# Performance work log

Hardware: AMD Instinct MI355X
Metric: run time of the kernel (lower is better)

The kernel has to match this reference:

```python
import jax, jax.numpy as jnp
import numpy as np

N_NODES = 50000
N_EDGES = 800000
F_IN = 512
HID = 256
N_CLS = 40
W_DIM = 50  # dimension*dimension*2 with dimension=5


def _prelu(x, a):
    return jnp.where(x >= 0, x, a * x)


def _segment_softmax(w, idx, n):
    # per-segment (grouped by idx), per-channel numerically stable softmax
    m = jax.ops.segment_max(w, idx, num_segments=n)
    e = jnp.exp(w - m[idx])
    s = jax.ops.segment_sum(e, idx, num_segments=n)
    return e / s[idx]


def _curvgn(x, edge_index, w_mul, W, b, w0, a, w1, b1):
    n = x.shape[0]
    h = x @ W + b                                   # [N, C]
    ow = _prelu(w_mul @ w0, a) @ w1 + b1            # [E, C] edge-weight MLP
    ow = _segment_softmax(ow, edge_index[0], n)     # softmax grouped by source (as in source)
    msg = ow * h[edge_index[0]]                     # gather x_j, weight
    return jax.ops.segment_sum(msg, edge_index[1], num_segments=n)  # scatter-add at target


def setup_inputs() -> dict:
    key = jax.random.key(0)
    ks = jax.random.split(key, 12)
    s = 0.05
    return {
        "x": jax.random.normal(ks[0], (N_NODES, F_IN), jnp.float32),
        "edge_index": jax.random.randint(ks[1], (2, N_EDGES), 0, N_NODES, jnp.int64 if jax.config.jax_enable_x64 else jnp.int32).astype(jnp.int32),
        "w_mul": jax.random.normal(ks[2], (N_EDGES, W_DIM), jnp.float32),
        "W1": jax.random.normal(ks[3], (F_IN, HID), jnp.float32) * s,
        "b1": jnp.zeros((HID,), jnp.float32),
        "m1_w0": jax.random.normal(ks[4], (W_DIM, HID), jnp.float32) * s,
        "m1_a": jnp.full((HID,), 0.2, jnp.float32),
        "m1_w1": jax.random.normal(ks[5], (HID, HID), jnp.float32) * s,
        "m1_b1": jnp.zeros((HID,), jnp.float32),
        "W2": jax.random.normal(ks[6], (HID, N_CLS), jnp.float32) * s,
        "b2": jnp.zeros((N_CLS,), jnp.float32),
        "m2_w0": jax.random.normal(ks[7], (W_DIM, N_CLS), jnp.float32) * s,
        "m2_a": jnp.full((N_CLS,), 0.2, jnp.float32),
        "m2_w1": jax.random.normal(ks[8], (N_CLS, N_CLS), jnp.float32) * s,
        "m2_b1": jnp.zeros((N_CLS,), jnp.float32),
    }


def reference(x, edge_index, w_mul, W1, b1, m1_w0, m1_a, m1_w1, m1_b1,
              W2, b2, m2_w0, m2_a, m2_w1, m2_b1):
    # eval mode: dropout is identity
    h = _curvgn(x, edge_index, w_mul, W1, b1, m1_w0, m1_a, m1_w1, m1_b1)
    h = jax.nn.elu(h)
    out = _curvgn(h, edge_index, w_mul, W2, b2, m2_w0, m2_a, m2_w1, m2_b1)
    return jax.nn.log_softmax(out, axis=1)
```

## Files before the change

kernel.cpp:

```cpp
#include <hip/hip_runtime.h>
#include <hip/hip_bf16.h>
#include <math.h>

#define N_NODESC 50000
#define N_EDGESC 800000
#define F_INC 512
#define HIDC 256
#define N_CLSC 40
#define W_DIMC 50
#define HN (2*N_NODESC)
#define NB_SCAN 196

typedef __bf16 bf16;
typedef __bf16 bf16x8 __attribute__((ext_vector_type(8)));
typedef __bf16 bf16x4 __attribute__((ext_vector_type(4)));
typedef __bf16 bf16x2 __attribute__((ext_vector_type(2)));
typedef float  f32x4  __attribute__((ext_vector_type(4)));
typedef float  f32x2  __attribute__((ext_vector_type(2)));

__global__ void k_hist(const int* __restrict__ ei, int* __restrict__ hist) {
    int e = blockIdx.x*256 + threadIdx.x;
    if (e < N_EDGESC) {
        atomicAdd(&hist[ei[e]], 1);
        atomicAdd(&hist[N_NODESC + ei[N_EDGESC + e]], 1);
    }
}
__global__ void k_copy(int* d, const int* s, int n) {
    int i = blockIdx.x*256 + threadIdx.x;
    if (i < n) d[i] = s[i];
}
__global__ void k_scan_part(const int* __restrict__ hist, int* __restrict__ part) {
    __shared__ int lds[512];
    int t = threadIdx.x;
    int i = blockIdx.x*512 + t;
    lds[t] = (i < HN) ? hist[i] : 0;
    __syncthreads();
    for (int off = 256; off > 0; off >>= 1) {
        if (t < off) lds[t] += lds[t+off];
        __syncthreads();
    }
    if (t == 0) part[blockIdx.x] = lds[0];
}
__global__ void k_scan_mid(const int* __restrict__ part, int* __restrict__ partx) {
    __shared__ int lds[256];
    int t = threadIdx.x;
    int v = (t < NB_SCAN) ? part[t] : 0;
    lds[t] = v;
    __syncthreads();
    for (int off = 1; off < 256; off <<= 1) {
        int add = (t >= off) ? lds[t-off] : 0;
        __syncthreads();
        lds[t] += add;
        __syncthreads();
    }
    partx[t] = lds[t] - v;
}
__global__ void k_scan_apply(const int* __restrict__ hist, const int* __restrict__ partx,
                             int* __restrict__ basev) {
    __shared__ int lds[512];
    int t = threadIdx.x;
    int i = blockIdx.x*512 + t;
    int v = (i < HN) ? hist[i] : 0;
    lds[t] = v;
    __syncthreads();
    for (int off = 1; off < 512; off <<= 1) {
        int add = (t >= off) ? lds[t-off] : 0;
        __syncthreads();
        lds[t] += add;
        __syncthreads();
    }
    if (i < HN) basev[i] = lds[t] - v + partx[blockIdx.x];
}
__global__ void k_scatter(const int* __restrict__ ei, int* __restrict__ cursor,
                          int* __restrict__ perm_src,
                          int* __restrict__ spd, int* __restrict__ svd) {
    int e = blockIdx.x*256 + threadIdx.x;
    if (e >= N_EDGESC) return;
    int s = ei[e];
    int d = ei[N_EDGESC + e];
    int p = atomicAdd(&cursor[s], 1);
    perm_src[p] = e;
    int q = atomicAdd(&cursor[N_NODESC + d], 1) - N_EDGESC;
    spd[q] = p;
    svd[q] = s;
}

__global__ void k_tconv(const float* __restrict__ src, bf16* __restrict__ dst,
                        int Ks, int Ns, int Kp, int Np) {
    int idx = blockIdx.x*256 + threadIdx.x;
    if (idx >= Kp*Np) return;
    int n = idx / Kp, k = idx - n*Kp;
    float v = (k < Ks && n < Ns) ? src[k*Ns + n] : 0.f;
    dst[idx] = (bf16)v;
}

__global__ __launch_bounds__(256) void k_h1(const float* __restrict__ x,
                                            const bf16* __restrict__ W1t,
                                            const float* __restrict__ b1,
                                            bf16* __restrict__ h1) {
    __shared__ __align__(16) bf16 a_lds[64*40];
    int tid = threadIdx.x;
    int lane = tid & 63, wv = tid >> 6;
    int l15 = lane & 15, quad = lane >> 4;
    int r0 = blockIdx.x * 64;
    f32x4 acc[4][4] = {};
    for (int ks = 0; ks < 16; ++ks) {
        #pragma unroll
        for (int i = 0; i < 2; ++i) {
            int idx = tid + i*256;
            int rl = idx >> 3, c4 = idx & 7;
            int rg = r0 + rl;
            f32x4 v = {};
            if (rg < N_NODESC) v = *(const f32x4*)&x[(size_t)rg*F_INC + ks*32 + c4*4];
            bf16x4 b; b[0]=(bf16)v[0]; b[1]=(bf16)v[1]; b[2]=(bf16)v[2]; b[3]=(bf16)v[3];
            *(bf16x4*)&a_lds[rl*40 + c4*4] = b;
        }
        __syncthreads();
        bf16x8 af[4], bfr[4];
        #pragma unroll
        for (int mt = 0; mt < 4; ++mt)
            af[mt] = *(const bf16x8*)&a_lds[(mt*16 + l15)*40 + quad*8];
        #pragma unroll
        for (int nt = 0; nt < 4; ++nt) {
            int n = wv*64 + nt*16 + l15;
            bfr[nt] = *(const bf16x8*)&W1t[n*F_INC + ks*32 + quad*8];
        }
        #pragma unroll
        for (int mt = 0; mt < 4; ++mt)
            #pragma unroll
            for (int nt = 0; nt < 4; ++nt)
                acc[mt][nt] = __builtin_amdgcn_mfma_f32_16x16x32_bf16(af[mt], bfr[nt], acc[mt][nt], 0, 0, 0);
        __syncthreads();
    }
    #pragma unroll
    for (int nt = 0; nt < 4; ++nt) {
        int col = wv*64 + nt*16 + l15;
        float bias = b1[col];
        #pragma unroll
        for (int mt = 0; mt < 4; ++mt)
            #pragma unroll
            for (int r = 0; r < 4; ++r) {
                int row = r0 + mt*16 + quad*4 + r;
                if (row < N_NODESC) h1[(size_t)row*HIDC + col] = (bf16)(acc[mt][nt][r] + bias);
            }
    }
}

__global__ __launch_bounds__(256) void k_mlp1(
    const float* __restrict__ w_mul, const int* __restrict__ perm_src,
    const int* __restrict__ ei,
    const bf16* __restrict__ w0t, const float* __restrict__ a1,
    const bf16* __restrict__ w1t, const float* __restrict__ bb1,
    bf16* __restrict__ eow1, float* __restrict__ s1) {
    __shared__ __align__(16) bf16 wm[64*72];
    __shared__ __align__(16) bf16 t1[64*264];
    __shared__ int e_lds[64], sv[64];
    int tid = threadIdx.x;
    int lane = tid & 63, wv = tid >> 6;
    int l15 = lane & 15, quad = lane >> 4;
    int p0 = blockIdx.x * 64;

    if (tid < 64) {
        int e = perm_src[p0 + tid];
        e_lds[tid] = e;
        sv[tid] = ei[e];
    }
    __syncthreads();
    #pragma unroll
    for (int i = 0; i < 7; ++i) {
        int idx = i*256 + tid;
        if (idx < 1600) {
            int row = idx / 25;
            int k = 2*(idx - row*25);
            f32x2 v = *(const f32x2*)&w_mul[(size_t)e_lds[row]*W_DIMC + k];
            bf16x2 b; b[0] = (bf16)v[0]; b[1] = (bf16)v[1];
            *(bf16x2*)&wm[row*72 + k] = b;
        }
    }
    #pragma unroll
    for (int i = 0; i < 2; ++i) {
        int idx = i*256 + tid;
        if (idx < 448) {
            int row = idx / 7, c = 50 + 2*(idx - row*7);
            bf16x2 z; z[0] = (bf16)0.f; z[1] = (bf16)0.f;
            *(bf16x2*)&wm[row*72 + c] = z;
        }
    }
    __syncthreads();

    {
        f32x4 acc[4][4] = {};
        bf16x8 af[2][4], bfr[2][4];
        #pragma unroll
        for (int ks = 0; ks < 2; ++ks) {
            #pragma unroll
            for (int mt = 0; mt < 4; ++mt)
                af[ks][mt] = *(const bf16x8*)&wm[(mt*16 + l15)*72 + ks*32 + quad*8];
            #pragma unroll
            for (int i = 0; i < 4; ++i)
                bfr[ks][i] = *(const bf16x8*)&w0t[(wv*64 + i*16 + l15)*64 + ks*32 + quad*8];
        }
        #pragma unroll
        for (int ks = 0; ks < 2; ++ks)
            #pragma unroll
            for (int mt = 0; mt < 4; ++mt)
                #pragma unroll
                for (int i = 0; i < 4; ++i)
                    acc[mt][i] = __builtin_amdgcn_mfma_f32_16x16x32_bf16(af[ks][mt], bfr[ks][i], acc[mt][i], 0, 0, 0);
        #pragma unroll
        for (int i = 0; i < 4; ++i) {
            int col = wv*64 + i*16 + l15;
            float al = a1[col];
            #pragma unroll
            for (int mt = 0; mt < 4; ++mt)
                #pragma unroll
                for (int r = 0; r < 4; ++r) {
                    float v = acc[mt][i][r];
                    v = (v >= 0.f) ? v : al*v;
                    t1[(mt*16 + quad*4 + r)*264 + col] = (bf16)v;
                }
        }
    }
    __syncthreads();

    {
        f32x4 acc[4][4] = {};
        bf16x8 af[2][4], bfr[2][4];
        #pragma unroll
        for (int mt = 0; mt < 4; ++mt)
            af[0][mt] = *(const bf16x8*)&t1[(mt*16 + l15)*264 + quad*8];
        #pragma unroll
        for (int i = 0; i < 4; ++i)
            bfr[0][i] = *(const bf16x8*)&w1t[(wv*64 + i*16 + l15)*HIDC + quad*8];
        #pragma unroll
        for (int ks = 0; ks < 8; ++ks) {
            int cur = ks & 1, nxt = cur ^ 1;
            if (ks < 7) {
                #pragma unroll
                for (int mt = 0; mt < 4; ++mt)
                    af[nxt][mt] = *(const bf16x8*)&t1[(mt*16 + l15)*264 + (ks+1)*32 + quad*8];
                #pragma unroll
                for (int i = 0; i < 4; ++i)
                    bfr[nxt][i] = *(const bf16x8*)&w1t[(wv*64 + i*16 + l15)*HIDC + (ks+1)*32 + quad*8];
            }
            #pragma unroll
            for (int mt = 0; mt < 4; ++mt)
                #pragma unroll
                for (int i = 0; i < 4; ++i)
                    acc[mt][i] = __builtin_amdgcn_mfma_f32_16x16x32_bf16(af[cur][mt], bfr[cur][i], acc[mt][i], 0, 0, 0);
        }
        __syncthreads();
        #pragma unroll
        for (int i = 0; i < 4; ++i) {
            int col = wv*64 + i*16 + l15;
            float bias = bb1[col];
            #pragma unroll
            for (int mt = 0; mt < 4; ++mt)
                #pragma unroll
                for (int r = 0; r < 4; ++r)
                    t1[(mt*16 + quad*4 + r)*264 + col] = (bf16)__expf(acc[mt][i][r] + bias);
        }
    }
    __syncthreads();

    #pragma unroll
    for (int i = 0; i < 8; ++i) {
        int idx = i*256 + tid;
        int row = idx >> 5, j = idx & 31;
        *(bf16x8*)&eow1[(size_t)(p0 + row)*HIDC + j*8] = *(const bf16x8*)&t1[row*264 + j*8];
    }
    {
        int c = tid;
        float acc2 = 0.f;
        #pragma unroll
        for (int r = 0; r < 64; ++r) {
            acc2 += (float)t1[r*264 + c];
            if (r == 63 || sv[r+1] != sv[r]) {
                atomicAdd(&s1[(size_t)sv[r]*HIDC + c], acc2);
                acc2 = 0.f;
            }
        }
    }
}

__global__ __launch_bounds__(256) void k_mlp2(
    const float* __restrict__ w_mul, const int* __restrict__ perm_src,
    const int* __restrict__ ei,
    const bf16* __restrict__ w20t, const float* __restrict__ a2,
    const bf16* __restrict__ w21t, const float* __restrict__ bb2,
    bf16* __restrict__ eow2, float* __restrict__ s2) {
    __shared__ __align__(16) bf16 wm[128*72];
    __shared__ __align__(16) bf16 t2[128*72];
    __shared__ int e_lds[128], sv[128];
    int tid = threadIdx.x;
    int lane = tid & 63, wv = tid >> 6;
    int l15 = lane & 15, quad = lane >> 4;
    int p0 = blockIdx.x * 128;

    if (tid < 128) {
        int e = perm_src[p0 + tid];
        e_lds[tid] = e;
        sv[tid] = ei[e];
    }
    __syncthreads();
    #pragma unroll
    for (int i = 0; i < 13; ++i) {
        int idx = i*256 + tid;
        if (idx < 3200) {
            int row = idx / 25;
            int k = 2*(idx - row*25);
            f32x2 v = *(const f32x2*)&w_mul[(size_t)e_lds[row]*W_DIMC + k];
            bf16x2 b; b[0] = (bf16)v[0]; b[1] = (bf16)v[1];
            *(bf16x2*)&wm[row*72 + k] = b;
        }
    }
    #pragma unroll
    for (int i = 0; i < 4; ++i) {
        int idx = i*256 + tid;
        if (idx < 896) {
            int row = idx / 7, c = 50 + 2*(idx - row*7);
            bf16x2 z; z[0] = (bf16)0.f; z[1] = (bf16)0.f;
            *(bf16x2*)&wm[row*72 + c] = z;
        }
    }
    #pragma unroll
    for (int i = 0; i < 4; ++i) {
        int idx = i*256 + tid;
        int row = idx >> 3, c = 48 + 2*(idx & 7);
        bf16x2 z; z[0] = (bf16)0.f; z[1] = (bf16)0.f;
        *(bf16x2*)&t2[row*72 + c] = z;
    }
    __syncthreads();

    {
        f32x4 acc[2][3] = {};
        #pragma unroll
        for (int ks = 0; ks < 2; ++ks) {
            bf16x8 af[2], bfr[3];
            #pragma unroll
            for (int mt = 0; mt < 2; ++mt)
                af[mt] = *(const bf16x8*)&wm[(wv*32 + mt*16 + l15)*72 + ks*32 + quad*8];
            #pragma unroll
            for (int i = 0; i < 3; ++i)
                bfr[i] = *(const bf16x8*)&w20t[(i*16 + l15)*64 + ks*32 + quad*8];
            #pragma unroll
            for (int mt = 0; mt < 2; ++mt)
                #pragma unroll
                for (int i = 0; i < 3; ++i)
                    acc[mt][i] = __builtin_amdgcn_mfma_f32_16x16x32_bf16(af[mt], bfr[i], acc[mt][i], 0, 0, 0);
        }
        #pragma unroll
        for (int i = 0; i < 3; ++i) {
            int col = i*16 + l15;
            float al = (col < N_CLSC) ? a2[col] : 0.f;
            #pragma unroll
            for (int mt = 0; mt < 2; ++mt)
                #pragma unroll
                for (int r = 0; r < 4; ++r) {
                    float v = acc[mt][i][r];
                    v = (v >= 0.f) ? v : al*v;
                    t2[(wv*32 + mt*16 + quad*4 + r)*72 + col] = (bf16)v;
                }
        }
    }

    {
        f32x4 acc[2][3] = {};
        #pragma unroll
        for (int ks = 0; ks < 2; ++ks) {
            bf16x8 af[2], bfr[3];
            #pragma unroll
            for (int mt = 0; mt < 2; ++mt)
                af[mt] = *(const bf16x8*)&t2[(wv*32 + mt*16 + l15)*72 + ks*32 + quad*8];
            #pragma unroll
            for (int i = 0; i < 3; ++i)
                bfr[i] = *(const bf16x8*)&w21t[(i*16 + l15)*64 + ks*32 + quad*8];
            #pragma unroll
            for (int mt = 0; mt < 2; ++mt)
                #pragma unroll
                for (int i = 0; i < 3; ++i)
                    acc[mt][i] = __builtin_amdgcn_mfma_f32_16x16x32_bf16(af[mt], bfr[i], acc[mt][i], 0, 0, 0);
        }
        #pragma unroll
        for (int i = 0; i < 3; ++i) {
            int col = i*16 + l15;
            if (col < N_CLSC) {
                float bias = bb2[col];
                #pragma unroll
                for (int mt = 0; mt < 2; ++mt)
                    #pragma unroll
                    for (int r = 0; r < 4; ++r)
                        t2[(wv*32 + mt*16 + quad*4 + r)*72 + col] = (bf16)__expf(acc[mt][i][r] + bias);
            }
        }
    }
    __syncthreads();

    #pragma unroll
    for (int i = 0; i < 3; ++i) {
        int idx = i*256 + tid;
        if (idx < 640) {
            int row = idx / 5, c8 = idx % 5;
            bf16x8 v = *(const bf16x8*)&t2[row*72 + c8*8];
            *(bf16x8*)&eow2[(size_t)(p0 + row)*N_CLSC + c8*8] = v;
        }
    }
    if (tid < 240) {
        int c = tid % 40, g = tid / 40;
        int rA = g*22, rB = (rA + 22 < 128) ? rA + 22 : 128;
        float acc = 0.f;
        for (int r = rA; r < rB; ++r) {
            acc += (float)t2[r*72 + c];
            if (r == rB-1 || sv[r+1] != sv[r]) {
                atomicAdd(&s2[(size_t)sv[r]*N_CLSC + c], acc);
                acc = 0.f;
            }
        }
    }
}

__global__ __launch_bounds__(256) void k_agg1(
    const bf16* __restrict__ eow1, const bf16* __restrict__ g1,
    const int* __restrict__ basev, const int* __restrict__ spd,
    const int* __restrict__ svd, float* __restrict__ out1) {
    int v = blockIdx.x, c = threadIdx.x;
    int b = basev[N_NODESC + v] - N_EDGESC;
    int e = (v < N_NODESC-1) ? basev[N_NODESC + v + 1] - N_EDGESC : N_EDGESC;
    float acc = 0.f;
    #pragma unroll 2
    for (int j = b; j < e; ++j) {
        int sp = spd[j], s = svd[j];
        acc += (float)eow1[(size_t)sp*HIDC + c] * (float)g1[(size_t)s*HIDC + c];
    }
    out1[(size_t)v*HIDC + c] = (acc > 0.f) ? acc : expm1f(acc);
}

__global__ __launch_bounds__(64) void k_agg2(
    const bf16* __restrict__ eow2, const bf16* __restrict__ g2,
    const int* __restrict__ basev, const int* __restrict__ spd,
    const int* __restrict__ svd, float* __restrict__ out) {
    int v = blockIdx.x, c = threadIdx.x;
    int b = basev[N_NODESC + v] - N_EDGESC;
    int e = (v < N_NODESC-1) ? basev[N_NODESC + v + 1] - N_EDGESC : N_EDGESC;
    bool act = (c < N_CLSC);
    float acc = 0.f;
    #pragma unroll 2
    for (int j = b; j < e; ++j) {
        int sp = spd[j], s = svd[j];
        if (act) acc += (float)eow2[(size_t)sp*N_CLSC + c] * (float)g2[(size_t)s*N_CLSC + c];
    }
    float m = act ? acc : -INFINITY;
    #pragma unroll
    for (int off = 32; off > 0; off >>= 1) m = fmaxf(m, __shfl_xor(m, off));
    float ex = act ? __expf(acc - m) : 0.f;
    #pragma unroll
    for (int off = 32; off > 0; off >>= 1) ex += __shfl_xor(ex, off);
    if (act) out[(size_t)v*N_CLSC + c] = acc - m - logf(ex);
}

__global__ void k_div_bf4(bf16* __restrict__ h, const float* __restrict__ s, int n4) {
    int i = blockIdx.x*256 + threadIdx.x;
    if (i < n4) {
        bf16x4 hv = *(bf16x4*)&h[i*4];
        f32x4 sv = *(const f32x4*)&s[i*4];
        #pragma unroll
        for (int k = 0; k < 4; ++k) hv[k] = (bf16)((float)hv[k] / sv[k]);
        *(bf16x4*)&h[i*4] = hv;
    }
}
__global__ void k_h2(const float* __restrict__ out1, const float* __restrict__ W2,
                     const float* __restrict__ b2, bf16* __restrict__ h2) {
    int i = blockIdx.x*256 + threadIdx.x;
    if (i >= N_NODESC*N_CLSC) return;
    int v = i / N_CLSC, c = i - v*N_CLSC;
    float acc = b2[c];
    const float* row = &out1[(size_t)v*HIDC];
    #pragma unroll 4
    for (int k = 0; k < HIDC; ++k) acc += row[k] * W2[k*N_CLSC + c];
    h2[i] = (bf16)acc;
}

extern "C" void kernel_launch(void* const* d_in, const int* in_sizes, int n_in,
                              void* d_out, int out_size, void* d_ws, size_t ws_size,
                              hipStream_t stream) {
    const float* x    = (const float*)d_in[0];
    const int*   ei   = (const int*)d_in[1];
    const float* wmul = (const float*)d_in[2];
    const float* W1   = (const float*)d_in[3];
    const float* b1   = (const float*)d_in[4];
    const float* m1w0 = (const float*)d_in[5];
    const float* m1a  = (const float*)d_in[6];
    const float* m1w1 = (const float*)d_in[7];
    const float* m1b1 = (const float*)d_in[8];
    const float* W2   = (const float*)d_in[9];
    const float* b2   = (const float*)d_in[10];
    const float* m2w0 = (const float*)d_in[11];
    const float* m2a  = (const float*)d_in[12];
    const float* m2w1 = (const float*)d_in[13];
    const float* m2b1 = (const float*)d_in[14];
    float* out = (float*)d_out;

    char* ws = (char*)d_ws;
    size_t off = 0;
    auto alloc = [&](size_t bytes) -> void* {
        off = (off + 255) & ~(size_t)255;
        void* p = ws + off;
        off += bytes;
        return p;
    };
    bf16*  h1g1  = (bf16*) alloc((size_t)N_NODESC*HIDC*2);
    float* s1o1  = (float*)alloc((size_t)N_NODESC*HIDC*4);
    bf16*  h2g2  = (bf16*) alloc((size_t)N_NODESC*N_CLSC*2);
    float* s2    = (float*)alloc((size_t)N_NODESC*N_CLSC*4);
    bf16*  W1t   = (bf16*) alloc(256*512*2);
    bf16*  w0t   = (bf16*) alloc(256*64*2);
    bf16*  w1tm  = (bf16*) alloc(256*256*2);
    bf16*  w20t  = (bf16*) alloc(48*64*2);
    bf16*  w21t  = (bf16*) alloc(48*64*2);
    int*   hist  = (int*)  alloc(HN*4);
    int*   basev = (int*)  alloc(HN*4);
    int*   cursor= (int*)  alloc(HN*4);
    int*   part  = (int*)  alloc(256*4);
    int*   partx = (int*)  alloc(256*4);
    int*   perm_src = (int*)alloc((size_t)N_EDGESC*4);
    int*   spd      = (int*)alloc((size_t)N_EDGESC*4);
    int*   svd      = (int*)alloc((size_t)N_EDGESC*4);
    bf16*  eow1  = (bf16*) alloc((size_t)N_EDGESC*HIDC*2);
    bf16*  eow2  = (bf16*) alloc((size_t)N_EDGESC*N_CLSC*2);

    hipMemsetAsync(hist, 0, HN*4, stream);
    hipMemsetAsync(s1o1, 0, (size_t)N_NODESC*HIDC*4, stream);
    hipMemsetAsync(s2,   0, (size_t)N_NODESC*N_CLSC*4, stream);
    k_hist<<<(N_EDGESC+255)/256, 256, 0, stream>>>(ei, hist);
    k_scan_part<<<NB_SCAN, 512, 0, stream>>>(hist, part);
    k_scan_mid<<<1, 256, 0, stream>>>(part, partx);
    k_scan_apply<<<NB_SCAN, 512, 0, stream>>>(hist, partx, basev);
    k_copy<<<(HN+255)/256, 256, 0, stream>>>(cursor, basev, HN);
    k_scatter<<<(N_EDGESC+255)/256, 256, 0, stream>>>(ei, cursor, perm_src, spd, svd);

    k_tconv<<<(512*256+255)/256, 256, 0, stream>>>(W1,   W1t, 512, 256, 512, 256);
    k_tconv<<<(256*64+255)/256,  256, 0, stream>>>(m1w0, w0t,  50, 256,  64, 256);
    k_tconv<<<(256*256+255)/256, 256, 0, stream>>>(m1w1, w1tm, 256, 256, 256, 256);
    k_tconv<<<(48*64+255)/256,   256, 0, stream>>>(m2w0, w20t,  50,  40,  64,  48);
    k_tconv<<<(48*64+255)/256,   256, 0, stream>>>(m2w1, w21t,  40,  40,  64,  48);

    k_h1<<<(N_NODESC+63)/64, 256, 0, stream>>>(x, W1t, b1, h1g1);
    k_mlp1<<<N_EDGESC/64, 256, 0, stream>>>(wmul, perm_src, ei, w0t, m1a, w1tm, m1b1,
                                            eow1, s1o1);
    k_mlp2<<<N_EDGESC/128, 256, 0, stream>>>(wmul, perm_src, ei, w20t, m2a, w21t, m2b1,
                                             eow2, s2);
    k_div_bf4<<<(N_NODESC*HIDC/4+255)/256, 256, 0, stream>>>(h1g1, s1o1, N_NODESC*HIDC/4);
    k_agg1<<<N_NODESC, 256, 0, stream>>>(eow1, h1g1, basev, spd, svd, s1o1);

    k_h2<<<(N_NODESC*N_CLSC+255)/256, 256, 0, stream>>>(s1o1, W2, b2, h2g2);
    k_div_bf4<<<(N_NODESC*N_CLSC/4+255)/256, 256, 0, stream>>>(h2g2, s2, N_NODESC*N_CLSC/4);
    k_agg2<<<N_NODESC, 64, 0, stream>>>(eow2, h2g2, basev, spd, svd, out);
}
```

Before: 1.501 ms.

## Gather edge MLP inputs directly into MFMA fragments and vectorize aggregation kernels

Both edge-MLP kernels now load w_mul rows straight from global memory into bf16 MFMA A-fragments instead of staging them through LDS, which removes a shared buffer and a barrier. k_mlp2 processes 256 edges per block with a tighter LDS stride. The segment-sum reduction in k_mlp1 uses 8-wide vector LDS reads with per-row-group atomics. k_agg1 uses 64 threads per node, each handling 4 channels with vector loads, which cuts the number of index loads per channel. The trade-off is more atomics in k_mlp1, since rows are split into groups, and uncoalesced direct global gathers.

```diff
diff --git a/kernel.cpp b/kernel.cpp
--- a/kernel.cpp
+++ b/kernel.cpp
@@ -146,13 +146,38 @@
     }
 }
 
-__global__ __launch_bounds__(256) void k_mlp1(
+__device__ __forceinline__ void gather_afrag(const float* __restrict__ w_mul,
+                                             int e, int quad,
+                                             bf16x8& a0, bf16x8& a1f) {
+    const float* rp = &w_mul[(size_t)e * W_DIMC];
+    {
+        f32x4 v0 = *(const f32x4*)&rp[quad*8];
+        f32x4 v1 = *(const f32x4*)&rp[quad*8 + 4];
+        a0[0]=(bf16)v0[0]; a0[1]=(bf16)v0[1]; a0[2]=(bf16)v0[2]; a0[3]=(bf16)v0[3];
+        a0[4]=(bf16)v1[0]; a0[5]=(bf16)v1[1]; a0[6]=(bf16)v1[2]; a0[7]=(bf16)v1[3];
+    }
+    if (quad < 2) {
+        f32x4 v0 = *(const f32x4*)&rp[32 + quad*8];
+        f32x4 v1 = *(const f32x4*)&rp[36 + quad*8];
+        a1f[0]=(bf16)v0[0]; a1f[1]=(bf16)v0[1]; a1f[2]=(bf16)v0[2]; a1f[3]=(bf16)v0[3];
+        a1f[4]=(bf16)v1[0]; a1f[5]=(bf16)v1[1]; a1f[6]=(bf16)v1[2]; a1f[7]=(bf16)v1[3];
+    } else if (quad == 2) {
+        f32x2 v = *(const f32x2*)&rp[48];
+        a1f[0]=(bf16)v[0]; a1f[1]=(bf16)v[1];
+        a1f[2]=(bf16)0.f; a1f[3]=(bf16)0.f; a1f[4]=(bf16)0.f;
+        a1f[5]=(bf16)0.f; a1f[6]=(bf16)0.f; a1f[7]=(bf16)0.f;
+    } else {
+        #pragma unroll
+        for (int k = 0; k < 8; ++k) a1f[k] = (bf16)0.f;
+    }
+}
+
+__global__ __launch_bounds__(256, 4) void k_mlp1(
     const float* __restrict__ w_mul, const int* __restrict__ perm_src,
     const int* __restrict__ ei,
     const bf16* __restrict__ w0t, const float* __restrict__ a1,
     const bf16* __restrict__ w1t, const float* __restrict__ bb1,
     bf16* __restrict__ eow1, float* __restrict__ s1) {
-    __shared__ __align__(16) bf16 wm[64*72];
     __shared__ __align__(16) bf16 t1[64*264];
     __shared__ int e_lds[64], sv[64];
     int tid = threadIdx.x;
@@ -166,40 +191,18 @@
         sv[tid] = ei[e];
     }
     __syncthreads();
-    #pragma unroll
-    for (int i = 0; i < 7; ++i) {
-        int idx = i*256 + tid;
-        if (idx < 1600) {
-            int row = idx / 25;
-            int k = 2*(idx - row*25);
-            f32x2 v = *(const f32x2*)&w_mul[(size_t)e_lds[row]*W_DIMC + k];
-            bf16x2 b; b[0] = (bf16)v[0]; b[1] = (bf16)v[1];
-            *(bf16x2*)&wm[row*72 + k] = b;
-        }
-    }
-    #pragma unroll
-    for (int i = 0; i < 2; ++i) {
-        int idx = i*256 + tid;
-        if (idx < 448) {
-            int row = idx / 7, c = 50 + 2*(idx - row*7);
-            bf16x2 z; z[0] = (bf16)0.f; z[1] = (bf16)0.f;
-            *(bf16x2*)&wm[row*72 + c] = z;
-        }
-    }
-    __syncthreads();
 
     {
         f32x4 acc[4][4] = {};
         bf16x8 af[2][4], bfr[2][4];
         #pragma unroll
-        for (int ks = 0; ks < 2; ++ks) {
-            #pragma unroll
-            for (int mt = 0; mt < 4; ++mt)
-                af[ks][mt] = *(const bf16x8*)&wm[(mt*16 + l15)*72 + ks*32 + quad*8];
+        for (int mt = 0; mt < 4; ++mt)
+            gather_afrag(w_mul, e_lds[mt*16 + l15], quad, af[0][mt], af[1][mt]);
+        #pragma unroll
+        for (int ks = 0; ks < 2; ++ks)
             #pragma unroll
             for (int i = 0; i < 4; ++i)
                 bfr[ks][i] = *(const bf16x8*)&w0t[(wv*64 + i*16 + l15)*64 + ks*32 + quad*8];
-        }
         #pragma unroll
         for (int ks = 0; ks < 2; ++ks)
             #pragma unroll
@@ -270,113 +273,97 @@
         *(bf16x8*)&eow1[(size_t)(p0 + row)*HIDC + j*8] = *(const bf16x8*)&t1[row*264 + j*8];
     }
     {
-        int c = tid;
-        float acc2 = 0.f;
-        #pragma unroll
-        for (int r = 0; r < 64; ++r) {
-            acc2 += (float)t1[r*264 + c];
-            if (r == 63 || sv[r+1] != sv[r]) {
-                atomicAdd(&s1[(size_t)sv[r]*HIDC + c], acc2);
-                acc2 = 0.f;
+        int c8 = tid & 31, g = tid >> 5;
+        float acc2[8] = {};
+        #pragma unroll
+        for (int r = g*8; r < g*8 + 8; ++r) {
+            bf16x8 v = *(const bf16x8*)&t1[r*264 + c8*8];
+            #pragma unroll
+            for (int k = 0; k < 8; ++k) acc2[k] += (float)v[k];
+            if (r == g*8 + 7 || sv[r+1] != sv[r]) {
+                float* dst = &s1[(size_t)sv[r]*HIDC + c8*8];
+                #pragma unroll
+                for (int k = 0; k < 8; ++k) atomicAdd(&dst[k], acc2[k]);
+                #pragma unroll
+                for (int k = 0; k < 8; ++k) acc2[k] = 0.f;
             }
         }
     }
 }
 
-__global__ __launch_bounds__(256) void k_mlp2(
+__global__ __launch_bounds__(256, 4) void k_mlp2(
     const float* __restrict__ w_mul, const int* __restrict__ perm_src,
     const int* __restrict__ ei,
     const bf16* __restrict__ w20t, const float* __restrict__ a2,
     const bf16* __restrict__ w21t, const float* __restrict__ bb2,
     bf16* __restrict__ eow2, float* __restrict__ s2) {
-    __shared__ __align__(16) bf16 wm[128*72];
-    __shared__ __align__(16) bf16 t2[128*72];
-    __shared__ int e_lds[128], sv[128];
+    __shared__ __align__(16) bf16 t2[256*68];
+    __shared__ int e_lds[256], sv[256];
     int tid = threadIdx.x;
     int lane = tid & 63, wv = tid >> 6;
     int l15 = lane & 15, quad = lane >> 4;
-    int p0 = blockIdx.x * 128;
-
-    if (tid < 128) {
+    int p0 = blockIdx.x * 256;
+
+    {
         int e = perm_src[p0 + tid];
         e_lds[tid] = e;
         sv[tid] = ei[e];
     }
-    __syncthreads();
-    #pragma unroll
-    for (int i = 0; i < 13; ++i) {
-        int idx = i*256 + tid;
-        if (idx < 3200) {
-            int row = idx / 25;
-            int k = 2*(idx - row*25);
-            f32x2 v = *(const f32x2*)&w_mul[(size_t)e_lds[row]*W_DIMC + k];
-            bf16x2 b; b[0] = (bf16)v[0]; b[1] = (bf16)v[1];
-            *(bf16x2*)&wm[row*72 + k] = b;
-        }
-    }
-    #pragma unroll
-    for (int i = 0; i < 4; ++i) {
-        int idx = i*256 + tid;
-        if (idx < 896) {
-            int row = idx / 7, c = 50 + 2*(idx - row*7);
-            bf16x2 z; z[0] = (bf16)0.f; z[1] = (bf16)0.f;
-            *(bf16x2*)&wm[row*72 + c] = z;
-        }
-    }
-    #pragma unroll
-    for (int i = 0; i < 4; ++i) {
-        int idx = i*256 + tid;
-        int row = idx >> 3, c = 48 + 2*(idx & 7);
+    #pragma unroll
+    for (int i = 0; i < 8; ++i) {
+        int idx = i*64 + lane;
+        int row = wv*64 + (idx >> 3), c = 48 + 2*(idx & 7);
         bf16x2 z; z[0] = (bf16)0.f; z[1] = (bf16)0.f;
-        *(bf16x2*)&t2[row*72 + c] = z;
-    }
-    __syncthreads();
-
-    {
-        f32x4 acc[2][3] = {};
-        #pragma unroll
-        for (int ks = 0; ks < 2; ++ks) {
-            bf16x8 af[2], bfr[3];
-            #pragma unroll
-            for (int mt = 0; mt < 2; ++mt)
-                af[mt] = *(const bf16x8*)&wm[(wv*32 + mt*16 + l15)*72 + ks*32 + quad*8];
+        *(bf16x2*)&t2[row*68 + c] = z;
+    }
+    __syncthreads();
+
+    {
+        f32x4 acc[4][3] = {};
+        bf16x8 af[2][4], bfr[2][3];
+        #pragma unroll
+        for (int mt = 0; mt < 4; ++mt)
+            gather_afrag(w_mul, e_lds[wv*64 + mt*16 + l15], quad, af[0][mt], af[1][mt]);
+        #pragma unroll
+        for (int ks = 0; ks < 2; ++ks)
             #pragma unroll
             for (int i = 0; i < 3; ++i)
-                bfr[i] = *(const bf16x8*)&w20t[(i*16 + l15)*64 + ks*32 + quad*8];
-            #pragma unroll
-            for (int mt = 0; mt < 2; ++mt)
+                bfr[ks][i] = *(const bf16x8*)&w20t[(i*16 + l15)*64 + ks*32 + quad*8];
+        #pragma unroll
+        for (int ks = 0; ks < 2; ++ks)
+            #pragma unroll
+            for (int mt = 0; mt < 4; ++mt)
                 #pragma unroll
                 for (int i = 0; i < 3; ++i)
-                    acc[mt][i] = __builtin_amdgcn_mfma_f32_16x16x32_bf16(af[mt], bfr[i], acc[mt][i], 0, 0, 0);
-        }
+                    acc[mt][i] = __builtin_amdgcn_mfma_f32_16x16x32_bf16(af[ks][mt], bfr[ks][i], acc[mt][i], 0, 0, 0);
         #pragma unroll
         for (int i = 0; i < 3; ++i) {
             int col = i*16 + l15;
             float al = (col < N_CLSC) ? a2[col] : 0.f;
             #pragma unroll
-            for (int mt = 0; mt < 2; ++mt)
+            for (int mt = 0; mt < 4; ++mt)
                 #pragma unroll
                 for (int r = 0; r < 4; ++r) {
                     float v = acc[mt][i][r];
                     v = (v >= 0.f) ? v : al*v;
-                    t2[(wv*32 + mt*16 + quad*4 + r)*72 + col] = (bf16)v;
+                    t2[(wv*64 + mt*16 + quad*4 + r)*68 + col] = (bf16)v;
                 }
         }
     }
 
     {
-        f32x4 acc[2][3] = {};
+        f32x4 acc[4][3] = {};
         #pragma unroll
         for (int ks = 0; ks < 2; ++ks) {
-            bf16x8 af[2], bfr[3];
-            #pragma unroll
-            for (int mt = 0; mt < 2; ++mt)
-                af[mt] = *(const bf16x8*)&t2[(wv*32 + mt*16 + l15)*72 + ks*32 + quad*8];
+            bf16x8 af[4], bfr[3];
+            #pragma unroll
+            for (int mt = 0; mt < 4; ++mt)
+                af[mt] = *(const bf16x8*)&t2[(wv*64 + mt*16 + l15)*68 + ks*32 + quad*8];
             #pragma unroll
             for (int i = 0; i < 3; ++i)
                 bfr[i] = *(const bf16x8*)&w21t[(i*16 + l15)*64 + ks*32 + quad*8];
             #pragma unroll
-            for (int mt = 0; mt < 2; ++mt)
+            for (int mt = 0; mt < 4; ++mt)
                 #pragma unroll
                 for (int i = 0; i < 3; ++i)
                     acc[mt][i] = __builtin_amdgcn_mfma_f32_16x16x32_bf16(af[mt], bfr[i], acc[mt][i], 0, 0, 0);
@@ -387,30 +374,28 @@
             if (col < N_CLSC) {
                 float bias = bb2[col];
                 #pragma unroll
-                for (int mt = 0; mt < 2; ++mt)
+                for (int mt = 0; mt < 4; ++mt)
                     #pragma unroll
                     for (int r = 0; r < 4; ++r)
-                        t2[(wv*32 + mt*16 + quad*4 + r)*72 + col] = (bf16)__expf(acc[mt][i][r] + bias);
+                        t2[(wv*64 + mt*16 + quad*4 + r)*68 + col] = (bf16)__expf(acc[mt][i][r] + bias);
             }
         }
     }
     __syncthreads();
 
     #pragma unroll
-    for (int i = 0; i < 3; ++i) {
+    for (int i = 0; i < 5; ++i) {
         int idx = i*256 + tid;
-        if (idx < 640) {
-            int row = idx / 5, c8 = idx % 5;
-            bf16x8 v = *(const bf16x8*)&t2[row*72 + c8*8];
-            *(bf16x8*)&eow2[(size_t)(p0 + row)*N_CLSC + c8*8] = v;
-        }
+        int row = idx / 5, c8 = idx % 5;
+        bf16x8 v = *(const bf16x8*)&t2[row*68 + c8*8];
+        *(bf16x8*)&eow2[(size_t)(p0 + row)*N_CLSC + c8*8] = v;
     }
     if (tid < 240) {
         int c = tid % 40, g = tid / 40;
-        int rA = g*22, rB = (rA + 22 < 128) ? rA + 22 : 128;
+        int rA = g*43, rB = (rA + 43 < 256) ? rA + 43 : 256;
         float acc = 0.f;
         for (int r = rA; r < rB; ++r) {
-            acc += (float)t2[r*72 + c];
+            acc += (float)t2[r*68 + c];
             if (r == rB-1 || sv[r+1] != sv[r]) {
                 atomicAdd(&s2[(size_t)sv[r]*N_CLSC + c], acc);
                 acc = 0.f;
@@ -419,20 +404,26 @@
     }
 }
 
-__global__ __launch_bounds__(256) void k_agg1(
+__global__ __launch_bounds__(64) void k_agg1(
     const bf16* __restrict__ eow1, const bf16* __restrict__ g1,
     const int* __restrict__ basev, const int* __restrict__ spd,
     const int* __restrict__ svd, float* __restrict__ out1) {
     int v = blockIdx.x, c = threadIdx.x;
     int b = basev[N_NODESC + v] - N_EDGESC;
     int e = (v < N_NODESC-1) ? basev[N_NODESC + v + 1] - N_EDGESC : N_EDGESC;
-    float acc = 0.f;
-    #pragma unroll 2
+    f32x4 acc = {};
+    #pragma unroll 4
     for (int j = b; j < e; ++j) {
         int sp = spd[j], s = svd[j];
-        acc += (float)eow1[(size_t)sp*HIDC + c] * (float)g1[(size_t)s*HIDC + c];
-    }
-    out1[(size_t)v*HIDC + c] = (acc > 0.f) ? acc : expm1f(acc);
+        bf16x4 ev = *(const bf16x4*)&eow1[(size_t)sp*HIDC + c*4];
+        bf16x4 gv = *(const bf16x4*)&g1[(size_t)s*HIDC + c*4];
+        #pragma unroll
+        for (int k = 0; k < 4; ++k) acc[k] += (float)ev[k] * (float)gv[k];
+    }
+    f32x4 o;
+    #pragma unroll
+    for (int k = 0; k < 4; ++k) o[k] = (acc[k] > 0.f) ? acc[k] : expm1f(acc[k]);
+    *(f32x4*)&out1[(size_t)v*HIDC + c*4] = o;
 }
 
 __global__ __launch_bounds__(64) void k_agg2(
@@ -547,10 +538,10 @@
     k_h1<<<(N_NODESC+63)/64, 256, 0, stream>>>(x, W1t, b1, h1g1);
     k_mlp1<<<N_EDGESC/64, 256, 0, stream>>>(wmul, perm_src, ei, w0t, m1a, w1tm, m1b1,
                                             eow1, s1o1);
-    k_mlp2<<<N_EDGESC/128, 256, 0, stream>>>(wmul, perm_src, ei, w20t, m2a, w21t, m2b1,
+    k_mlp2<<<N_EDGESC/256, 256, 0, stream>>>(wmul, perm_src, ei, w20t, m2a, w21t, m2b1,
                                              eow2, s2);
     k_div_bf4<<<(N_NODESC*HIDC/4+255)/256, 256, 0, stream>>>(h1g1, s1o1, N_NODESC*HIDC/4);
-    k_agg1<<<N_NODESC, 256, 0, stream>>>(eow1, h1g1, basev, spd, svd, s1o1);
+    k_agg1<<<N_NODESC, 64, 0, stream>>>(eow1, h1g1, basev, spd, svd, s1o1);
 
     k_h2<<<(N_NODESC*N_CLSC+255)/256, 256, 0, stream>>>(s1o1, W2, b2, h2g2);
     k_div_bf4<<<(N_NODESC*N_CLSC/4+255)/256, 256, 0, stream>>>(h2g2, s2, N_NODESC*N_CLSC/4);
```

Result: slower. 2.266 ms (+50.9%).
